# Kernel tuning notes

Measured on AMD Instinct MI355X. Metric: run time of the kernel, lower is better.

## Reference

```python
import jax, jax.numpy as jnp
import numpy as np

NW, NT = 200000, 100000
DW, DT = 128, 64
HID, HEADS, OUT = 64, 2, 2
HC = HID * HEADS  # 128
E = 500000
NEG_SLOPE = 0.2


def setup_inputs() -> dict:
    key = jax.random.key(0)
    ks = iter(jax.random.split(key, 40))

    def nrm(shape, scale):
        return jax.random.normal(next(ks), shape, dtype=jnp.float32) * scale

    inp = {
        "x_wallet": nrm((NW, DW), 1.0),
        "x_token": nrm((NT, DT), 1.0),
        # per-node-type input projections Linear(in, hidden)
        "lin_w_W": nrm((DW, HID), 1.0 / np.sqrt(DW)),
        "lin_w_b": jnp.zeros((HID,), jnp.float32),
        "lin_t_W": nrm((DT, HID), 1.0 / np.sqrt(DT)),
        "lin_t_b": jnp.zeros((HID,), jnp.float32),
        # GAT layer 0: in=HID(64) -> H*C(128), stacked over 3 edge types
        "Wsrc0": nrm((3, HID, HC), 1.0 / np.sqrt(HID)),
        "Wdst0": nrm((3, HID, HC), 1.0 / np.sqrt(HID)),
        "atts0": nrm((3, HEADS, HID), 1.0 / np.sqrt(HID)),
        "attd0": nrm((3, HEADS, HID), 1.0 / np.sqrt(HID)),
        "b0": jnp.zeros((3, HC), jnp.float32),
        # GAT layer 1: in=H*C(128) -> H*C(128)
        "Wsrc1": nrm((3, HC, HC), 1.0 / np.sqrt(HC)),
        "Wdst1": nrm((3, HC, HC), 1.0 / np.sqrt(HC)),
        "atts1": nrm((3, HEADS, HID), 1.0 / np.sqrt(HID)),
        "attd1": nrm((3, HEADS, HID), 1.0 / np.sqrt(HID)),
        "b1": jnp.zeros((3, HC), jnp.float32),
        # classifiers Linear(H*C, out)
        "cls_w_W": nrm((HC, OUT), 1.0 / np.sqrt(HC)),
        "cls_w_b": jnp.zeros((OUT,), jnp.float32),
        "cls_t_W": nrm((HC, OUT), 1.0 / np.sqrt(HC)),
        "cls_t_b": jnp.zeros((OUT,), jnp.float32),
        # edge indices: [2, E] with row0 = src ids, row1 = dst ids
        "e_wt": jnp.stack([jax.random.randint(next(ks), (E,), 0, NW),
                            jax.random.randint(next(ks), (E,), 0, NT)]).astype(jnp.int64),
        "e_tw": jnp.stack([jax.random.randint(next(ks), (E,), 0, NT),
                            jax.random.randint(next(ks), (E,), 0, NW)]).astype(jnp.int64),
        "e_ww": jnp.stack([jax.random.randint(next(ks), (E,), 0, NW),
                            jax.random.randint(next(ks), (E,), 0, NW)]).astype(jnp.int64),
    }
    return inp


def gat_conv(x_src, x_dst, edge, Wsrc, Wdst, att_s, att_d, bias, n_dst):
    # bipartite GATConv: project, per-edge attention, segment softmax over dst, scatter-sum
    hs = (x_src @ Wsrc).reshape(-1, HEADS, HID)  # [Ns,H,C]
    hd = (x_dst @ Wdst).reshape(-1, HEADS, HID)  # [Nd,H,C]
    a_s = jnp.einsum("nhc,hc->nh", hs, att_s)    # [Ns,H]
    a_d = jnp.einsum("nhc,hc->nh", hd, att_d)    # [Nd,H]
    s, d = edge[0], edge[1]
    alpha = jax.nn.leaky_relu(a_s[s] + a_d[d], NEG_SLOPE)  # [E,H]
    m = jax.ops.segment_max(alpha, d, num_segments=n_dst)
    m = jnp.where(jnp.isfinite(m), m, 0.0)  # nodes with no in-edges
    ex = jnp.exp(alpha - m[d])
    den = jax.ops.segment_sum(ex, d, num_segments=n_dst)
    alpha = ex / (den[d] + 1e-16)
    out = jax.ops.segment_sum(alpha[:, :, None] * hs[s], d, num_segments=n_dst)  # [Nd,H,C]
    return out.reshape(n_dst, HC) + bias


def reference(x_wallet, x_token, lin_w_W, lin_w_b, lin_t_W, lin_t_b,
              Wsrc0, Wdst0, atts0, attd0, b0,
              Wsrc1, Wdst1, atts1, attd1, b1,
              cls_w_W, cls_w_b, cls_t_W, cls_t_b,
              e_wt, e_tw, e_ww):
    xw = x_wallet @ lin_w_W + lin_w_b
    xt = x_token @ lin_t_W + lin_t_b
    for Wsrc, Wdst, ats, atd, b in ((Wsrc0, Wdst0, atts0, attd0, b0),
                                     (Wsrc1, Wdst1, atts1, attd1, b1)):
        # edge type 0: wallet->token, 1: token->wallet, 2: wallet->wallet; HeteroConv aggr='sum'
        out_t = gat_conv(xw, xt, e_wt, Wsrc[0], Wdst[0], ats[0], atd[0], b[0], NT)
        out_w = (gat_conv(xt, xw, e_tw, Wsrc[1], Wdst[1], ats[1], atd[1], b[1], NW)
                 + gat_conv(xw, xw, e_ww, Wsrc[2], Wdst[2], ats[2], atd[2], b[2], NW))
        xw = jax.nn.elu(out_w)
        xt = jax.nn.elu(out_t)
    logits_w = xw @ cls_w_W + cls_w_b  # [NW,2]
    logits_t = xt @ cls_t_W + cls_t_b  # [NT,2]
    return jnp.concatenate([logits_w, logits_t], axis=0)  # [NW+NT,2]
```

## Files before the change

kernel.cpp:

```cpp
#include <hip/hip_runtime.h>
#include <stdint.h>

typedef unsigned short ushort_t;
typedef short s8v __attribute__((ext_vector_type(8)));
typedef float f4v __attribute__((ext_vector_type(4)));

#define NW 200000
#define NT 100000
#define EE 500000
#define NSEG (NT + NW + NW)

__device__ __forceinline__ float b2f(unsigned short u){
  union { unsigned int i; float f; } v; v.i = ((unsigned int)u) << 16; return v.f;
}
__device__ __forceinline__ unsigned short f2b(float f){
  unsigned int x = __float_as_uint(f);
  unsigned int r = x + 0x7fffu + ((x >> 16) & 1u);
  return (unsigned short)(r >> 16);
}
__device__ __forceinline__ float ldf(const void* p, long idx, int fm){
  return fm ? ((const float*)p)[idx] : b2f(((const ushort_t*)p)[idx]);
}

__global__ void detect_kern(const int* ewt, const int* etw, const int* eww,
                            const unsigned* xw_words, int* mode){
  if (threadIdx.x == 0 && blockIdx.x == 0){
    unsigned o = 0;
    for (int i = 0; i < 64; ++i)
      o |= (unsigned)ewt[2 * i + 1] | (unsigned)etw[2 * i + 1] | (unsigned)eww[2 * i + 1];
    mode[0] = (o == 0) ? 1 : 0;
    int viol = 0;
    for (int i = 0; i < 256; ++i){
      unsigned s = xw_words[i] & 0xffffu;
      unsigned e = (s >> 7) & 0xffu;
      if (!(s == 0u || s == 0x8000u || (e >= 90u && e <= 140u))) viol++;
    }
    mode[1] = (viol > 8) ? 1 : 0;
  }
}

struct TDesc { const void* src; ushort_t* dst; long ebase; int K; int N; };
struct TDesc8 { TDesc d[8]; };
__global__ void transpose8(TDesc8 td, const int* mode){
  int fm = mode[1];
  int mi = blockIdx.x >> 6;
  TDesc t = td.d[mi];
  int e = ((blockIdx.x & 63) << 8) + threadIdx.x;
  if (e < t.K * t.N){
    int k = e / t.N, n = e - k * t.N;
    t.dst[n * t.K + k] = f2b(ldf(t.src, t.ebase + e, fm));
  }
}

__global__ void uprep(const void* Wsrc0, const void* Wdst0, const void* atts0, const void* attd0,
                      const void* Wsrc1, const void* Wdst1, const void* atts1, const void* attd1,
                      float* Uw0, float* Ut0, float* Uw1, float* Ut1, const int* mode){
  int fm = mode[1];
  int id = blockIdx.x * 256 + threadIdx.x;
  if (id >= (64 + 128) * 12) return;
  int layer = (id >= 64 * 12);
  int rem = layer ? id - 64 * 12 : id;
  int K = layer ? 128 : 64;
  int k = rem / 12, j = rem % 12;
  const void* Ws = layer ? Wsrc1 : Wsrc0;
  const void* Wd = layer ? Wdst1 : Wdst0;
  const void* As = layer ? atts1 : atts0;
  const void* Ad = layer ? attd1 : attd0;
  int t, h; bool src;
  if (j < 8){ const int tt[8] = {0,0,2,2,1,1,2,2}; t = tt[j]; h = j & 1; src = (j < 4); }
  else { int jj = j - 8; t = (jj < 2) ? 1 : 0; h = jj & 1; src = (jj < 2); }
  const void* W = src ? Ws : Wd;
  const void* A = src ? As : Ad;
  float acc = 0.f;
  for (int c = 0; c < 64; ++c)
    acc += ldf(W, (long)(t * K + k) * 128 + h * 64 + c, fm) * ldf(A, t * 128 + h * 64 + c, fm);
  if (j < 8) (layer ? Uw1 : Uw0)[k * 8 + j] = acc;
  else       (layer ? Ut1 : Ut0)[k * 4 + (j - 8)] = acc;
}

__global__ void hist_kern(const int* ewt, const int* etw, const int* eww, const int* mode, int* deg){
  int i = blockIdx.x * 256 + threadIdx.x;
  if (i >= 3 * EE) return;
  int md = mode[0];
  int t = i / EE, e = i - t * EE;
  const int* ep = (t == 0) ? ewt : (t == 1) ? etw : eww;
  int d = md ? ep[2 * (EE + e)] : ep[EE + e];
  int base = (t == 0) ? 0 : (t == 1) ? NT : NT + NW;
  atomicAdd(&deg[base + d], 1);
}

__global__ __launch_bounds__(512) void scan1(const int* deg, int* excl, int* sums){
  __shared__ int pair[512];
  int t = threadIdx.x;
  int base = blockIdx.x * 1024;
  int i0 = base + 2 * t;
  int a = (i0 < NSEG) ? deg[i0] : 0;
  int b = (i0 + 1 < NSEG) ? deg[i0 + 1] : 0;
  int ps = a + b;
  pair[t] = ps;
  __syncthreads();
  for (int off = 1; off < 512; off <<= 1){
    int v = (t >= off) ? pair[t - off] : 0;
    __syncthreads();
    if (t >= off) pair[t] += v;
    __syncthreads();
  }
  int epair = pair[t] - ps;
  if (i0 < NSEG) excl[i0] = epair;
  if (i0 + 1 < NSEG) excl[i0 + 1] = epair + a;
  if (t == 511) sums[blockIdx.x] = pair[511];
}

__global__ __launch_bounds__(512) void scan2(int* sums, int nch){
  __shared__ int s[512];
  int t = threadIdx.x;
  int orig = (t < nch) ? sums[t] : 0;
  s[t] = orig;
  __syncthreads();
  for (int off = 1; off < 512; off <<= 1){
    int v = (t >= off) ? s[t - off] : 0;
    __syncthreads();
    if (t >= off) s[t] += v;
    __syncthreads();
  }
  if (t < nch) sums[t] = s[t] - orig;
}

__global__ void scan3(int* rowptr, int* cursor, const int* sums){
  int i = blockIdx.x * 256 + threadIdx.x;
  if (i < NSEG){
    int v = rowptr[i] + sums[i >> 10];
    rowptr[i] = v; cursor[i] = v;
  }
  if (i == 0) rowptr[NSEG] = 3 * EE;
}

__global__ void fill_kern(const int* ewt, const int* etw, const int* eww, const int* mode,
                          int* cursor, int* adj){
  int i = blockIdx.x * 256 + threadIdx.x;
  if (i >= 3 * EE) return;
  int md = mode[0];
  int t = i / EE, e = i - t * EE;
  const int* ep = (t == 0) ? ewt : (t == 1) ? etw : eww;
  int s = md ? ep[2 * e] : ep[e];
  int d = md ? ep[2 * (EE + e)] : ep[EE + e];
  int base = (t == 0) ? 0 : (t == 1) ? NT : NT + NW;
  int pos = atomicAdd(&cursor[base + d], 1);
  adj[pos] = s;
}

template<int K, int NC, bool BIAS, bool EXTA>
__global__ __launch_bounds__(256, 2) void gemm_kern(const void* __restrict__ A, const ushort_t* __restrict__ Bt,
    const void* __restrict__ bias, ushort_t* __restrict__ C, int M,
    const int* __restrict__ mode, int nchunk){
  constexpr int CT = NC / 16, KK = K / 32;
  int fm = EXTA ? mode[1] : 0;
  int tid = threadIdx.x, lane = tid & 63, wave = tid >> 6;
  int rl = lane & 15, kq = (lane >> 4) * 8;
  s8v bfrag[CT][KK];
#pragma unroll
  for (int ct = 0; ct < CT; ++ct)
#pragma unroll
    for (int kk = 0; kk < KK; ++kk)
      bfrag[ct][kk] = *(const s8v*)(Bt + (long)(ct * 16 + rl) * K + kk * 32 + kq);
  float biasv[CT];
  if (BIAS){
#pragma unroll
    for (int ct = 0; ct < CT; ++ct) biasv[ct] = ldf(bias, ct * 16 + rl, fm);
  }
  for (int chunk = blockIdx.x; chunk < nchunk; chunk += gridDim.x){
    long m0 = (long)chunk * 128 + wave * 32;
    f4v acc[2][CT];
#pragma unroll
    for (int rt = 0; rt < 2; ++rt)
#pragma unroll
      for (int ct = 0; ct < CT; ++ct) acc[rt][ct] = (f4v){0.f, 0.f, 0.f, 0.f};
#pragma unroll
    for (int rt = 0; rt < 2; ++rt){
      long row = m0 + rt * 16 + rl;
      bool ok = row < (long)M;
#pragma unroll
      for (int kk = 0; kk < KK; ++kk){
        s8v a = (s8v){0,0,0,0,0,0,0,0};
        if (ok){
          long e = row * K + kk * 32 + kq;
          if (EXTA && fm){
            const float* p = (const float*)A + e;
            uint4 lo = *(const uint4*)p;
            uint4 hi = *(const uint4*)(p + 4);
            union { s8v v; unsigned u[4]; } t;
            t.u[0] = (unsigned)f2b(__uint_as_float(lo.x)) | ((unsigned)f2b(__uint_as_float(lo.y)) << 16);
            t.u[1] = (unsigned)f2b(__uint_as_float(lo.z)) | ((unsigned)f2b(__uint_as_float(lo.w)) << 16);
            t.u[2] = (unsigned)f2b(__uint_as_float(hi.x)) | ((unsigned)f2b(__uint_as_float(hi.y)) << 16);
            t.u[3] = (unsigned)f2b(__uint_as_float(hi.z)) | ((unsigned)f2b(__uint_as_float(hi.w)) << 16);
            a = t.v;
          } else {
            a = *(const s8v*)((const ushort_t*)A + e);
          }
        }
#pragma unroll
        for (int ct = 0; ct < CT; ++ct)
          acc[rt][ct] = __builtin_amdgcn_mfma_f32_16x16x32_bf16(a, bfrag[ct][kk], acc[rt][ct], 0, 0, 0);
      }
    }
#pragma unroll
    for (int rt = 0; rt < 2; ++rt){
      long rbase = (long)chunk * 128 + wave * 32 + rt * 16 + (lane >> 4) * 4;
#pragma unroll
      for (int ct = 0; ct < CT; ++ct){
#pragma unroll
        for (int r = 0; r < 4; ++r){
          long gm = rbase + r;
          if (gm < (long)M){
            float v = acc[rt][ct][r];
            if (BIAS) v += biasv[ct];
            C[gm * NC + ct * 16 + rl] = f2b(v);
          }
        }
      }
    }
  }
}

template<int K, int NCOL>
__global__ __launch_bounds__(256) void a_kern(const ushort_t* __restrict__ x, const float* __restrict__ U,
                                              float* __restrict__ out, int N){
  int n = blockIdx.x * 256 + threadIdx.x;
  if (n >= N) return;
  float acc[NCOL];
#pragma unroll
  for (int j = 0; j < NCOL; ++j) acc[j] = 0.f;
  const ushort_t* xr = x + (long)n * K;
#pragma unroll
  for (int k8 = 0; k8 < K / 8; ++k8){
    uint4 v = *(const uint4*)(xr + k8 * 8);
    unsigned uu[4] = {v.x, v.y, v.z, v.w};
#pragma unroll
    for (int i = 0; i < 4; ++i){
      float f0 = b2f((unsigned short)(uu[i] & 0xffffu));
      float f1 = b2f((unsigned short)(uu[i] >> 16));
      const float* Ur = U + (k8 * 8 + i * 2) * NCOL;
#pragma unroll
      for (int j = 0; j < NCOL; ++j) acc[j] += f0 * Ur[j] + f1 * Ur[NCOL + j];
    }
  }
  f4v* o4 = (f4v*)(out + (long)n * NCOL);
#pragma unroll
  for (int q = 0; q < NCOL / 4; ++q){
    f4v t = {acc[q * 4], acc[q * 4 + 1], acc[q * 4 + 2], acc[q * 4 + 3]};
    o4[q] = t;
  }
}

__device__ __forceinline__ void round_load(const int* __restrict__ adj,
    const float* __restrict__ asrc, int stride, int col, int j, int cnt,
    const ushort_t* __restrict__ hs, int c0, float2 (&av)[8], unsigned (&h)[8]){
#pragma unroll
  for (int i = 0; i < 8; ++i){
    if (i < cnt){
      int s = adj[j + i];
      av[i] = *(const float2*)(asrc + (long)s * stride + col);
      h[i] = *(const unsigned*)(hs + (long)s * 128 + c0);
    }
  }
}

__device__ __forceinline__ void round_acc(int cnt, float adl, int hi,
    const float2 (&av)[8], const unsigned (&h)[8],
    float& n0, float& n1, float& den, float& mm){
  float al[8];
  float rm = -1e30f;
#pragma unroll
  for (int i = 0; i < 8; ++i){
    if (i < cnt){
      float x = (hi ? av[i].y : av[i].x) + adl;
      x = x > 0.f ? x : 0.2f * x;
      al[i] = x;
      rm = fmaxf(rm, x);
    }
  }
  float mnew = fmaxf(mm, rm);
  float sc = __expf(mm - mnew);
  n0 *= sc; n1 *= sc; den *= sc; mm = mnew;
#pragma unroll
  for (int i = 0; i < 8; ++i){
    if (i < cnt){
      float e = __expf(al[i] - mnew);
      den += e;
      n0 += e * b2f((unsigned short)(h[i] & 0xffffu));
      n1 += e * b2f((unsigned short)(h[i] >> 16));
    }
  }
}

template<bool FINAL>
__global__ __launch_bounds__(256) void agg_all(const int* __restrict__ rowptr, const int* __restrict__ adj,
    const float* __restrict__ aw, const float* __restrict__ at,
    const ushort_t* __restrict__ hs0, const ushort_t* __restrict__ hs1, const ushort_t* __restrict__ hs2,
    const void* __restrict__ bsrc, ushort_t* __restrict__ xt_out, ushort_t* __restrict__ xw_out,
    const void* __restrict__ clsWw, const void* __restrict__ clsbw,
    const void* __restrict__ clsWt, const void* __restrict__ clsbt,
    void* __restrict__ dout, const int* __restrict__ mode){
  int fm = mode[1];
  int wv = __builtin_amdgcn_readfirstlane(threadIdx.x >> 6);
  int lane = threadIdx.x & 63;
  int hi = lane >> 5;
  int c0 = lane << 1;
  int bid = blockIdx.x;
  const int TB = NT / 4;
  bool is_tok = bid < TB;
  float o0, o1;
  int d;
  if (is_tok){
    d = bid * 4 + wv;
    float2 ad = *(const float2*)(at + (long)d * 4 + 2);
    float adl = hi ? ad.y : ad.x;
    int beg = rowptr[d], end = rowptr[d + 1];
    float n0 = 0.f, n1 = 0.f, den = 0.f, mm = -1e30f;
    for (int j = beg; j < end; j += 8){
      int cnt = min(end - j, 8);
      float2 av[8]; unsigned h[8];
      round_load(adj, aw, 8, 0, j, cnt, hs0, c0, av, h);
      round_acc(cnt, adl, hi, av, h, n0, n1, den, mm);
    }
    float inv = 1.f / (den + 1e-16f);
    o0 = n0 * inv + ldf(bsrc, c0, fm);
    o1 = n1 * inv + ldf(bsrc, c0 + 1, fm);
  } else {
    d = (bid - TB) * 4 + wv;
    float2 ad1 = *(const float2*)(aw + (long)d * 8 + 4);
    float2 ad2 = *(const float2*)(aw + (long)d * 8 + 6);
    float adl1 = hi ? ad1.y : ad1.x;
    float adl2 = hi ? ad2.y : ad2.x;
    int s1 = NT + d, s2 = NT + NW + d;
    int b1 = rowptr[s1], e1 = rowptr[s1 + 1];
    int b2 = rowptr[s2], e2 = rowptr[s2 + 1];
    int c1 = min(e1 - b1, 8), c2 = min(e2 - b2, 8);
    float n10 = 0.f, n11 = 0.f, den1 = 0.f, mm1 = -1e30f;
    float n20 = 0.f, n21 = 0.f, den2 = 0.f, mm2 = -1e30f;
    {
      float2 av1[8], av2[8]; unsigned h1[8], h2[8];
      if (c1 > 0) round_load(adj, at, 4, 0, b1, c1, hs1, c0, av1, h1);
      if (c2 > 0) round_load(adj, aw, 8, 2, b2, c2, hs2, c0, av2, h2);
      if (c1 > 0) round_acc(c1, adl1, hi, av1, h1, n10, n11, den1, mm1);
      if (c2 > 0) round_acc(c2, adl2, hi, av2, h2, n20, n21, den2, mm2);
    }
    for (int j = b1 + 8; j < e1; j += 8){
      int cnt = min(e1 - j, 8);
      float2 av[8]; unsigned h[8];
      round_load(adj, at, 4, 0, j, cnt, hs1, c0, av, h);
      round_acc(cnt, adl1, hi, av, h, n10, n11, den1, mm1);
    }
    for (int j = b2 + 8; j < e2; j += 8){
      int cnt = min(e2 - j, 8);
      float2 av[8]; unsigned h[8];
      round_load(adj, aw, 8, 2, j, cnt, hs2, c0, av, h);
      round_acc(cnt, adl2, hi, av, h, n20, n21, den2, mm2);
    }
    float i1v = 1.f / (den1 + 1e-16f), i2v = 1.f / (den2 + 1e-16f);
    o0 = n10 * i1v + n20 * i2v + ldf(bsrc, 128 + c0, fm)     + ldf(bsrc, 256 + c0, fm);
    o1 = n11 * i1v + n21 * i2v + ldf(bsrc, 128 + c0 + 1, fm) + ldf(bsrc, 256 + c0 + 1, fm);
  }
  o0 = o0 > 0.f ? o0 : __expf(o0) - 1.f;
  o1 = o1 > 0.f ? o1 : __expf(o1) - 1.f;
  if (!FINAL){
    ushort_t* out = is_tok ? xt_out : xw_out;
    unsigned pack = (unsigned)f2b(o0) | ((unsigned)f2b(o1) << 16);
    *(unsigned*)(out + (long)d * 128 + c0) = pack;
  } else {
    const void* W = is_tok ? clsWt : clsWw;
    const void* b = is_tok ? clsbt : clsbw;
    float w00 = ldf(W, 4 * lane + 0, fm), w01 = ldf(W, 4 * lane + 1, fm);
    float w10 = ldf(W, 4 * lane + 2, fm), w11 = ldf(W, 4 * lane + 3, fm);
    float p0 = o0 * w00 + o1 * w10;
    float p1 = o0 * w01 + o1 * w11;
#pragma unroll
    for (int off = 32; off > 0; off >>= 1){ p0 += __shfl_xor(p0, off, 64); p1 += __shfl_xor(p1, off, 64); }
    if (lane == 0){
      long g = is_tok ? (long)NW + d : (long)d;
      float r0 = p0 + ldf(b, 0, fm);
      float r1 = p1 + ldf(b, 1, fm);
      if (fm){ ((float*)dout)[g * 2] = r0; ((float*)dout)[g * 2 + 1] = r1; }
      else { ((ushort_t*)dout)[g * 2] = f2b(r0); ((ushort_t*)dout)[g * 2 + 1] = f2b(r1); }
    }
  }
}

extern "C" void kernel_launch(void* const* d_in, const int* in_sizes, int n_in,
                              void* d_out, int out_size, void* d_ws, size_t ws_size,
                              hipStream_t stream){
  const void* x_wallet = d_in[0];
  const void* x_token  = d_in[1];
  const void* lin_w_W  = d_in[2];
  const void* lin_w_b  = d_in[3];
  const void* lin_t_W  = d_in[4];
  const void* lin_t_b  = d_in[5];
  const void* Wsrc0    = d_in[6];
  const void* Wdst0    = d_in[7];
  const void* atts0    = d_in[8];
  const void* attd0    = d_in[9];
  const void* b0       = d_in[10];
  const void* Wsrc1    = d_in[11];
  const void* Wdst1    = d_in[12];
  const void* atts1    = d_in[13];
  const void* attd1    = d_in[14];
  const void* b1       = d_in[15];
  const void* cls_w_W  = d_in[16];
  const void* cls_w_b  = d_in[17];
  const void* cls_t_W  = d_in[18];
  const void* cls_t_b  = d_in[19];
  const int* e_wt = (const int*)d_in[20];
  const int* e_tw = (const int*)d_in[21];
  const int* e_ww = (const int*)d_in[22];

  char* ws = (char*)d_ws;
  size_t off = 0;
  auto alloc = [&](size_t bytes) -> char* {
    char* p = ws + off; off += (bytes + 255) & ~(size_t)255; return p;
  };
  int* rowptr = (int*)alloc((size_t)(NSEG + 1) * 4);
  int* deg    = (int*)alloc((size_t)(NSEG + 1) * 4);
  int* adj    = (int*)alloc((size_t)3 * EE * 4);
  int* sums   = (int*)alloc(512 * 4);
  int* mode   = (int*)alloc(8);
  ushort_t* BtLw = (ushort_t*)alloc(64 * 128 * 2);
  ushort_t* BtLt = (ushort_t*)alloc(64 * 64 * 2);
  ushort_t* BtS0 = (ushort_t*)alloc(3 * 128 * 64 * 2);
  ushort_t* BtS1 = (ushort_t*)alloc(3 * 128 * 128 * 2);
  float* Uw0 = (float*)alloc(64 * 8 * 4);
  float* Ut0 = (float*)alloc(64 * 4 * 4);
  float* Uw1 = (float*)alloc(128 * 8 * 4);
  float* Ut1 = (float*)alloc(128 * 4 * 4);
  float* aw = (float*)alloc((size_t)NW * 8 * 4);
  float* at = (float*)alloc((size_t)NT * 4 * 4);
  ushort_t* hs0 = (ushort_t*)alloc((size_t)NW * 128 * 2);
  ushort_t* hs1 = (ushort_t*)alloc((size_t)NT * 128 * 2);
  ushort_t* hs2 = (ushort_t*)alloc((size_t)NW * 128 * 2);
  ushort_t* xbuf = (ushort_t*)alloc(((size_t)NW + NT) * 128 * 2);
  ushort_t* xw0 = xbuf;
  ushort_t* xt0 = xbuf + (size_t)NW * 64;
  ushort_t* xwB = xbuf;
  ushort_t* xtB = xbuf + (size_t)NW * 128;
  (void)in_sizes; (void)n_in;

  if (off > ws_size){
    hipMemsetAsync(d_out, 0, (size_t)out_size * 2, stream);
    return;
  }

  hipMemsetAsync(deg, 0, (size_t)NSEG * 4, stream);
  detect_kern<<<1, 64, 0, stream>>>(e_wt, e_tw, e_ww, (const unsigned*)x_wallet, mode);

  TDesc8 td;
  td.d[0] = { lin_w_W, BtLw, 0, 128, 64 };
  td.d[1] = { lin_t_W, BtLt, 0, 64, 64 };
  for (int t = 0; t < 3; ++t){
    td.d[2 + t] = { Wsrc0, BtS0 + t * 128 * 64,  (long)t * 64 * 128,  64,  128 };
    td.d[5 + t] = { Wsrc1, BtS1 + t * 128 * 128, (long)t * 128 * 128, 128, 128 };
  }
  transpose8<<<512, 256, 0, stream>>>(td, mode);
  uprep<<<9, 256, 0, stream>>>(Wsrc0, Wdst0, atts0, attd0, Wsrc1, Wdst1, atts1, attd1, Uw0, Ut0, Uw1, Ut1, mode);

  int egrid = (3 * EE + 255) / 256;
  hist_kern<<<egrid, 256, 0, stream>>>(e_wt, e_tw, e_ww, mode, deg);
  int nch = (NSEG + 1023) / 1024;
  scan1<<<nch, 512, 0, stream>>>(deg, rowptr, sums);
  scan2<<<1, 512, 0, stream>>>(sums, nch);
  scan3<<<(NSEG + 255) / 256, 256, 0, stream>>>(rowptr, deg, sums);
  fill_kern<<<egrid, 256, 0, stream>>>(e_wt, e_tw, e_ww, mode, deg, adj);

  const int G = 512;
  int ncW = (NW + 127) / 128, ncT = (NT + 127) / 128;
  int agrid = NT / 4 + NW / 4;

  gemm_kern<128, 64, true, true><<<G, 256, 0, stream>>>(x_wallet, BtLw, lin_w_b, xw0, NW, mode, ncW);
  gemm_kern<64, 64, true, true><<<G, 256, 0, stream>>>(x_token, BtLt, lin_t_b, xt0, NT, mode, ncT);

  a_kern<64, 8><<<(NW + 255) / 256, 256, 0, stream>>>(xw0, Uw0, aw, NW);
  a_kern<64, 4><<<(NT + 255) / 256, 256, 0, stream>>>(xt0, Ut0, at, NT);
  gemm_kern<64, 128, false, false><<<G, 256, 0, stream>>>(xw0, BtS0, nullptr, hs0, NW, mode, ncW);
  gemm_kern<64, 128, false, false><<<G, 256, 0, stream>>>(xt0, BtS0 + 128 * 64, nullptr, hs1, NT, mode, ncT);
  gemm_kern<64, 128, false, false><<<G, 256, 0, stream>>>(xw0, BtS0 + 2 * 128 * 64, nullptr, hs2, NW, mode, ncW);
  agg_all<false><<<agrid, 256, 0, stream>>>(rowptr, adj, aw, at, hs0, hs1, hs2, b0, xtB, xwB,
                                            nullptr, nullptr, nullptr, nullptr, nullptr, mode);

  a_kern<128, 8><<<(NW + 255) / 256, 256, 0, stream>>>(xwB, Uw1, aw, NW);
  a_kern<128, 4><<<(NT + 255) / 256, 256, 0, stream>>>(xtB, Ut1, at, NT);
  gemm_kern<128, 128, false, false><<<G, 256, 0, stream>>>(xwB, BtS1, nullptr, hs0, NW, mode, ncW);
  gemm_kern<128, 128, false, false><<<G, 256, 0, stream>>>(xtB, BtS1 + 128 * 128, nullptr, hs1, NT, mode, ncT);
  gemm_kern<128, 128, false, false><<<G, 256, 0, stream>>>(xwB, BtS1 + 2 * 128 * 128, nullptr, hs2, NW, mode, ncW);
  agg_all<true><<<agrid, 256, 0, stream>>>(rowptr, adj, aw, at, hs0, hs1, hs2, b1, nullptr, nullptr,
                                           cls_w_W, cls_w_b, cls_t_W, cls_t_b, d_out, mode);
}
```

Baseline: 924.7 us.

## Precompute per-node exponentials to replace online softmax with products

The per-node attention projection kernel now stores exp(a) and exp(0.2a) for every source and destination score. Each edge weight is then formed as a product of these factors, choosing the branch that matches the LeakyReLU sign test. This removes the per-edge exp calls and the running-max rescaling from the aggregation loops. In exchange the attention buffers double in size, and the softmax is no longer max-shifted, so large logits could overflow.

```diff
diff --git a/kernel.cpp b/kernel.cpp
--- a/kernel.cpp
+++ b/kernel.cpp
@@ -244,51 +244,38 @@
       for (int j = 0; j < NCOL; ++j) acc[j] += f0 * Ur[j] + f1 * Ur[NCOL + j];
     }
   }
-  f4v* o4 = (f4v*)(out + (long)n * NCOL);
-#pragma unroll
-  for (int q = 0; q < NCOL / 4; ++q){
-    f4v t = {acc[q * 4], acc[q * 4 + 1], acc[q * 4 + 2], acc[q * 4 + 3]};
-    o4[q] = t;
+  float* o = out + (long)n * (2 * NCOL);
+#pragma unroll
+  for (int q = 0; q < NCOL / 2; ++q){
+    f4v t = {__expf(acc[2 * q]), __expf(0.2f * acc[2 * q]),
+             __expf(acc[2 * q + 1]), __expf(0.2f * acc[2 * q + 1])};
+    *(f4v*)(o + q * 4) = t;
   }
 }
 
 __device__ __forceinline__ void round_load(const int* __restrict__ adj,
-    const float* __restrict__ asrc, int stride, int col, int j, int cnt,
-    const ushort_t* __restrict__ hs, int c0, float2 (&av)[8], unsigned (&h)[8]){
+    const float* __restrict__ psrc, int sstr, int j, int cnt,
+    const ushort_t* __restrict__ hb, float2 (&pq)[8], unsigned (&h)[8]){
 #pragma unroll
   for (int i = 0; i < 8; ++i){
     if (i < cnt){
       int s = adj[j + i];
-      av[i] = *(const float2*)(asrc + (long)s * stride + col);
-      h[i] = *(const unsigned*)(hs + (long)s * 128 + c0);
-    }
-  }
-}
-
-__device__ __forceinline__ void round_acc(int cnt, float adl, int hi,
-    const float2 (&av)[8], const unsigned (&h)[8],
-    float& n0, float& n1, float& den, float& mm){
-  float al[8];
-  float rm = -1e30f;
+      pq[i] = *(const float2*)(psrc + (long)s * sstr);
+      h[i] = *(const unsigned*)(hb + (long)s * 128);
+    }
+  }
+}
+
+__device__ __forceinline__ void round_acc(int cnt, float pd, float qd,
+    const float2 (&pq)[8], const unsigned (&h)[8], float& n0, float& n1, float& den){
 #pragma unroll
   for (int i = 0; i < 8; ++i){
     if (i < cnt){
-      float x = (hi ? av[i].y : av[i].x) + adl;
-      x = x > 0.f ? x : 0.2f * x;
-      al[i] = x;
-      rm = fmaxf(rm, x);
-    }
-  }
-  float mnew = fmaxf(mm, rm);
-  float sc = __expf(mm - mnew);
-  n0 *= sc; n1 *= sc; den *= sc; mm = mnew;
-#pragma unroll
-  for (int i = 0; i < 8; ++i){
-    if (i < cnt){
-      float e = __expf(al[i] - mnew);
-      den += e;
-      n0 += e * b2f((unsigned short)(h[i] & 0xffffu));
-      n1 += e * b2f((unsigned short)(h[i] >> 16));
+      float t = pq[i].x * pd, u = pq[i].y * qd;
+      float w = t > 1.f ? t : u;
+      den += w;
+      n0 += w * b2f((unsigned short)(h[i] & 0xffffu));
+      n1 += w * b2f((unsigned short)(h[i] >> 16));
     }
   }
 }
@@ -304,7 +291,7 @@
   int fm = mode[1];
   int wv = __builtin_amdgcn_readfirstlane(threadIdx.x >> 6);
   int lane = threadIdx.x & 63;
-  int hi = lane >> 5;
+  int hh = lane >> 5;
   int c0 = lane << 1;
   int bid = blockIdx.x;
   const int TB = NT / 4;
@@ -313,49 +300,53 @@
   int d;
   if (is_tok){
     d = bid * 4 + wv;
-    float2 ad = *(const float2*)(at + (long)d * 4 + 2);
-    float adl = hi ? ad.y : ad.x;
+    float2 dq = *(const float2*)(at + (long)d * 8 + 4 + hh * 2);
+    const float* ps = aw + hh * 2;
+    const ushort_t* hb = hs0 + c0;
     int beg = rowptr[d], end = rowptr[d + 1];
-    float n0 = 0.f, n1 = 0.f, den = 0.f, mm = -1e30f;
+    float n0 = 0.f, n1 = 0.f, den = 0.f;
     for (int j = beg; j < end; j += 8){
       int cnt = min(end - j, 8);
-      float2 av[8]; unsigned h[8];
-      round_load(adj, aw, 8, 0, j, cnt, hs0, c0, av, h);
-      round_acc(cnt, adl, hi, av, h, n0, n1, den, mm);
+      float2 pq[8]; unsigned h[8];
+      round_load(adj, ps, 16, j, cnt, hb, pq, h);
+      round_acc(cnt, dq.x, dq.y, pq, h, n0, n1, den);
     }
     float inv = 1.f / (den + 1e-16f);
     o0 = n0 * inv + ldf(bsrc, c0, fm);
     o1 = n1 * inv + ldf(bsrc, c0 + 1, fm);
   } else {
     d = (bid - TB) * 4 + wv;
-    float2 ad1 = *(const float2*)(aw + (long)d * 8 + 4);
-    float2 ad2 = *(const float2*)(aw + (long)d * 8 + 6);
-    float adl1 = hi ? ad1.y : ad1.x;
-    float adl2 = hi ? ad2.y : ad2.x;
+    const float* awd = aw + (long)d * 16;
+    float2 dq1 = *(const float2*)(awd + 8 + hh * 2);
+    float2 dq2 = *(const float2*)(awd + 12 + hh * 2);
+    const float* ps1 = at + hh * 2;
+    const float* ps2 = aw + 4 + hh * 2;
+    const ushort_t* hb1 = hs1 + c0;
+    const ushort_t* hb2 = hs2 + c0;
     int s1 = NT + d, s2 = NT + NW + d;
     int b1 = rowptr[s1], e1 = rowptr[s1 + 1];
     int b2 = rowptr[s2], e2 = rowptr[s2 + 1];
     int c1 = min(e1 - b1, 8), c2 = min(e2 - b2, 8);
-    float n10 = 0.f, n11 = 0.f, den1 = 0.f, mm1 = -1e30f;
-    float n20 = 0.f, n21 = 0.f, den2 = 0.f, mm2 = -1e30f;
+    float n10 = 0.f, n11 = 0.f, den1 = 0.f;
+    float n20 = 0.f, n21 = 0.f, den2 = 0.f;
     {
-      float2 av1[8], av2[8]; unsigned h1[8], h2[8];
-      if (c1 > 0) round_load(adj, at, 4, 0, b1, c1, hs1, c0, av1, h1);
-      if (c2 > 0) round_load(adj, aw, 8, 2, b2, c2, hs2, c0, av2, h2);
-      if (c1 > 0) round_acc(c1, adl1, hi, av1, h1, n10, n11, den1, mm1);
-      if (c2 > 0) round_acc(c2, adl2, hi, av2, h2, n20, n21, den2, mm2);
+      float2 pq1[8], pq2[8]; unsigned h1[8], h2[8];
+      if (c1 > 0) round_load(adj, ps1, 8, b1, c1, hb1, pq1, h1);
+      if (c2 > 0) round_load(adj, ps2, 16, b2, c2, hb2, pq2, h2);
+      if (c1 > 0) round_acc(c1, dq1.x, dq1.y, pq1, h1, n10, n11, den1);
+      if (c2 > 0) round_acc(c2, dq2.x, dq2.y, pq2, h2, n20, n21, den2);
     }
     for (int j = b1 + 8; j < e1; j += 8){
       int cnt = min(e1 - j, 8);
-      float2 av[8]; unsigned h[8];
-      round_load(adj, at, 4, 0, j, cnt, hs1, c0, av, h);
-      round_acc(cnt, adl1, hi, av, h, n10, n11, den1, mm1);
+      float2 pq[8]; unsigned h[8];
+      round_load(adj, ps1, 8, j, cnt, hb1, pq, h);
+      round_acc(cnt, dq1.x, dq1.y, pq, h, n10, n11, den1);
     }
     for (int j = b2 + 8; j < e2; j += 8){
       int cnt = min(e2 - j, 8);
-      float2 av[8]; unsigned h[8];
-      round_load(adj, aw, 8, 2, j, cnt, hs2, c0, av, h);
-      round_acc(cnt, adl2, hi, av, h, n20, n21, den2, mm2);
+      float2 pq[8]; unsigned h[8];
+      round_load(adj, ps2, 16, j, cnt, hb2, pq, h);
+      round_acc(cnt, dq2.x, dq2.y, pq, h, n20, n21, den2);
     }
     float i1v = 1.f / (den1 + 1e-16f), i2v = 1.f / (den2 + 1e-16f);
     o0 = n10 * i1v + n20 * i2v + ldf(bsrc, 128 + c0, fm)     + ldf(bsrc, 256 + c0, fm);
@@ -431,8 +422,8 @@
   float* Ut0 = (float*)alloc(64 * 4 * 4);
   float* Uw1 = (float*)alloc(128 * 8 * 4);
   float* Ut1 = (float*)alloc(128 * 4 * 4);
-  float* aw = (float*)alloc((size_t)NW * 8 * 4);
-  float* at = (float*)alloc((size_t)NT * 4 * 4);
+  float* aw = (float*)alloc((size_t)NW * 16 * 4);
+  float* at = (float*)alloc((size_t)NT * 8 * 4);
   ushort_t* hs0 = (ushort_t*)alloc((size_t)NW * 128 * 2);
   ushort_t* hs1 = (ushort_t*)alloc((size_t)NT * 128 * 2);
   ushort_t* hs2 = (ushort_t*)alloc((size_t)NW * 128 * 2);
```

After: 934.5 us. No clear change (+1.1%).
